# Kernel optimization log

Hardware: AMD Instinct MI355X
Metric: run time of the kernel (lower is better)

The kernel has to match this reference:

```python
import jax, jax.numpy as jnp
import numpy as np

N_NODES = 100000
N_EDGES = 1600000
F_IN = 92
E_IN = 50
D = 64
N_LAYERS = 3
N_GRAPHS = 512
BN_EPS = 1e-5


def setup_inputs() -> dict:
    key = jax.random.key(0)
    ks = jax.random.split(key, 24)
    s = 0.05
    inp = {
        'x': jax.random.normal(ks[0], (N_NODES, F_IN), jnp.float32),
        'edge_index': jax.random.randint(ks[1], (2, N_EDGES), 0, N_NODES, jnp.int64),
        'edge_attr': jax.random.normal(ks[2], (N_EDGES, E_IN), jnp.float32),
        'batch_idx': jnp.sort(jax.random.randint(ks[3], (N_NODES,), 0, N_GRAPHS, jnp.int64)),
        'pre_w': jax.random.normal(ks[4], (F_IN, D), jnp.float32) * s,
        'pre_b': jax.random.normal(ks[5], (D,), jnp.float32) * s,
        'Wk': jax.random.normal(ks[6], (N_LAYERS, D, D), jnp.float32) * s,
        'bk': jax.random.normal(ks[7], (N_LAYERS, D), jnp.float32) * s,
        'Wq': jax.random.normal(ks[8], (N_LAYERS, D, D), jnp.float32) * s,
        'bq': jax.random.normal(ks[9], (N_LAYERS, D), jnp.float32) * s,
        'Wv': jax.random.normal(ks[10], (N_LAYERS, D, D), jnp.float32) * s,
        'bv': jax.random.normal(ks[11], (N_LAYERS, D), jnp.float32) * s,
        'We': jax.random.normal(ks[12], (N_LAYERS, E_IN, D), jnp.float32) * s,
        'Wskip': jax.random.normal(ks[13], (N_LAYERS, D, D), jnp.float32) * s,
        'conv_bias': jax.random.normal(ks[14], (N_LAYERS, D), jnp.float32) * s,
        'bn_gamma': jnp.ones((N_LAYERS, D), jnp.float32),
        'bn_beta': jnp.zeros((N_LAYERS, D), jnp.float32),
        'post_w': jax.random.normal(ks[15], (D, D), jnp.float32) * s,
        'post_b': jax.random.normal(ks[16], (D,), jnp.float32) * s,
        'out_w': jax.random.normal(ks[17], (D, 1), jnp.float32) * s,
        'out_b': jax.random.normal(ks[18], (1,), jnp.float32) * s,
        'num_graphs': N_GRAPHS,
    }
    return inp


def _forward(x, edge_index, edge_attr, batch_idx, pre_w, pre_b, Wk, bk, Wq, bq, Wv, bv,
             We, Wskip, conv_bias, bn_gamma, bn_beta, post_w, post_b, out_w, out_b, num_graphs):
    n_nodes = x.shape[0]
    src, dst = edge_index[0], edge_index[1]  # j -> i, aggregate at i=dst
    # pre-FC + silu
    h = jax.nn.silu(x @ pre_w + pre_b)
    for l in range(Wk.shape[0]):
        # ResGatedGraphConv: node-level projections first (dense GEMMs)
        k = h @ Wk[l] + bk[l]   # key, used at target i
        q = h @ Wq[l] + bq[l]   # query, used at source j
        v = h @ Wv[l] + bv[l]   # value, used at source j
        e = edge_attr @ We[l]   # [E, D] edge embedding (no bias)
        # gather-gate-scatter over edges
        gate = jax.nn.silu((k[dst] + e) + (q[src] + e))  # act = silu
        msg = gate * (v[src] + e)                         # [E, D]
        agg = jax.ops.segment_sum(msg, dst, num_segments=n_nodes)
        h = agg + h @ Wskip[l] + conv_bias[l]
        # BatchNorm1d (training-mode batch stats, biased variance)
        mean = jnp.mean(h, axis=0)
        var = jnp.var(h, axis=0)
        h = (h - mean) * jax.lax.rsqrt(var + BN_EPS) * bn_gamma[l] + bn_beta[l]
        # dropout_rate = 0.0 -> no-op
    # global_mean_pool (early)
    sums = jax.ops.segment_sum(h, batch_idx, num_segments=num_graphs)
    cnts = jax.ops.segment_sum(jnp.ones((n_nodes,), h.dtype), batch_idx, num_segments=num_graphs)
    g = sums / jnp.maximum(cnts, 1.0)[:, None]
    g = jax.nn.silu(g @ post_w + post_b)
    out = g @ out_w + out_b  # [G, 1]
    return out.reshape(-1)


def reference(x, edge_index, edge_attr, batch_idx, pre_w, pre_b, Wk, bk, Wq, bq, Wv, bv,
              We, Wskip, conv_bias, bn_gamma, bn_beta, post_w, post_b, out_w, out_b, num_graphs):
    return _forward(x, edge_index, edge_attr, batch_idx, pre_w, pre_b, Wk, bk, Wq, bq, Wv, bv,
                    We, Wskip, conv_bias, bn_gamma, bn_beta, post_w, post_b, out_w, out_b, num_graphs)
```

## Files before the change

### kernel.cpp

```cpp
#include <hip/hip_runtime.h>
#include <math.h>

#define N_NODES 100000
#define N_EDGES 1600000
#define F_IN 92
#define E_IN 50
#define D 64
#define N_LAYERS 3
#define N_GRAPHS 512
#define BN_EPS 1e-5f

#define SCAN_BLK 1024
#define SCAN_NCH ((N_NODES + SCAN_BLK - 1) / SCAN_BLK)
#define EMB_TILE 256

__device__ __forceinline__ float silu_f(float x) {
    return x / (1.0f + __expf(-x));
}

__device__ __forceinline__ float bcast_f(float v, int lane) {
    return __int_as_float(__builtin_amdgcn_readlane(__float_as_int(v), lane));
}

__global__ __launch_bounds__(256) void deg_within_kernel(
    const int* __restrict__ dst, int* __restrict__ deg, int* __restrict__ within) {
    for (int e = blockIdx.x * 256 + threadIdx.x; e < N_EDGES; e += gridDim.x * 256)
        within[e] = atomicAdd(&deg[dst[e]], 1);
}

__global__ __launch_bounds__(SCAN_BLK) void scan_sum_kernel(
    const int* __restrict__ deg, int* __restrict__ partials) {
    int b = blockIdx.x, t = threadIdx.x;
    int i = b * SCAN_BLK + t;
    int v = (i < N_NODES) ? deg[i] : 0;
    __shared__ int wsum[16];
    for (int off = 32; off > 0; off >>= 1) v += __shfl_down(v, off);
    if ((t & 63) == 0) wsum[t >> 6] = v;
    __syncthreads();
    if (t < 16) {
        int s = wsum[t];
        for (int off = 8; off > 0; off >>= 1) s += __shfl_down(s, off);
        if (t == 0) partials[b] = s;
    }
}

__global__ __launch_bounds__(128) void scan_part_kernel(int* __restrict__ partials) {
    int t = threadIdx.x;
    __shared__ int sh[128];
    sh[t] = (t < SCAN_NCH) ? partials[t] : 0;
    __syncthreads();
    for (int off = 1; off < 128; off <<= 1) {
        int v = (t >= off) ? sh[t - off] : 0;
        __syncthreads();
        sh[t] += v;
        __syncthreads();
    }
    if (t < SCAN_NCH) partials[t] = (t == 0) ? 0 : sh[t - 1];
}

__global__ __launch_bounds__(SCAN_BLK) void scan_write_kernel(
    const int* __restrict__ deg, const int* __restrict__ partials,
    int* __restrict__ row_start, int* __restrict__ cursor) {
    int b = blockIdx.x, t = threadIdx.x;
    int i = b * SCAN_BLK + t;
    int v = (i < N_NODES) ? deg[i] : 0;
    __shared__ int sh[SCAN_BLK];
    sh[t] = v;
    __syncthreads();
    for (int off = 1; off < SCAN_BLK; off <<= 1) {
        int x = (t >= off) ? sh[t - off] : 0;
        __syncthreads();
        sh[t] += x;
        __syncthreads();
    }
    int excl = partials[b] + sh[t] - v;
    if (i < N_NODES) { row_start[i] = excl; cursor[i] = excl; }
    if (i == N_NODES - 1) row_start[N_NODES] = excl + v;
}

__global__ __launch_bounds__(256) void pos_fin_kernel(
    const int* __restrict__ srcIdx, const int* __restrict__ dst,
    const int* __restrict__ row_start, int* __restrict__ pos_arr,
    int* __restrict__ src_s) {
    for (int e = blockIdx.x * 256 + threadIdx.x; e < N_EDGES; e += gridDim.x * 256) {
        int p = row_start[dst[e]] + pos_arr[e];
        pos_arr[e] = p;
        src_s[p] = srcIdx[e];
    }
}

__global__ __launch_bounds__(256) void scatter_kernel(
    const int* __restrict__ dst, int* __restrict__ cursor,
    int* __restrict__ csr) {
    for (int e = blockIdx.x * 256 + threadIdx.x; e < N_EDGES; e += gridDim.x * 256) {
        int pos = atomicAdd(&cursor[dst[e]], 1);
        csr[pos] = e;
    }
}

template <int STRIDE>
__global__ __launch_bounds__(256) void scatter_perm_kernel(
    const int* __restrict__ srcIdx, const int* __restrict__ dstIdx,
    const float* __restrict__ ea, int* __restrict__ cursor,
    float* __restrict__ ea_s, int* __restrict__ src_s) {
    int d = threadIdx.x;
    int e = blockIdx.x * 4 + threadIdx.y;
    if (e >= N_EDGES) return;
    int pos = 0;
    if (d == 0) pos = atomicAdd(&cursor[dstIdx[e]], 1);
    pos = __builtin_amdgcn_readlane(pos, 0);
    if (d == 0) src_s[pos] = srcIdx[e];
    if (d < E_IN) ea_s[(long)pos * STRIDE + d] = ea[(long)e * E_IN + d];
}

__global__ __launch_bounds__(256) void pre_fc_kernel(
    const float* __restrict__ x, const float* __restrict__ w,
    const float* __restrict__ b, float* __restrict__ h) {
    __shared__ float xs[4][F_IN];
    int d = threadIdx.x, yy = threadIdx.y;
    int node = blockIdx.x * 4 + yy;
    if (node < N_NODES) {
        const float* xrow = x + (long)node * F_IN;
        for (int i = d; i < F_IN; i += 64) xs[yy][i] = xrow[i];
    }
    __syncthreads();
    if (node >= N_NODES) return;
    float acc = b[d];
#pragma unroll 4
    for (int i = 0; i < F_IN; ++i) acc = fmaf(xs[yy][i], w[i * D + d], acc);
    h[(long)node * D + d] = silu_f(acc);
}

template <bool BN>
__global__ __launch_bounds__(256) void proj_kernel(
    const float* __restrict__ hin, const float* __restrict__ stats,
    const float* __restrict__ gamma, const float* __restrict__ beta,
    const float* __restrict__ Wk, const float* __restrict__ bk,
    const float* __restrict__ Wq, const float* __restrict__ bq,
    const float* __restrict__ Wv, const float* __restrict__ bv,
    const float* __restrict__ Ws, const float* __restrict__ cbias,
    float* __restrict__ ko, float* __restrict__ qo, float* __restrict__ vo,
    float* __restrict__ hnew) {
    __shared__ float hs[4][D];
    int d = threadIdx.x, yy = threadIdx.y;
    int node = blockIdx.x * 4 + yy;
    if (node < N_NODES) {
        float xv = hin[(long)node * D + d];
        if (BN) {
            const float invN = 1.0f / (float)N_NODES;
            float mean = stats[d] * invN;
            float var = stats[D + d] * invN - mean * mean;
            float sc = rsqrtf(var + BN_EPS) * gamma[d];
            xv = (xv - mean) * sc + beta[d];
        }
        hs[yy][d] = xv;
    }
    __syncthreads();
    if (node >= N_NODES) return;
    float ak = bk[d], aq = bq[d], av = bv[d], as = cbias[d];
#pragma unroll 8
    for (int i = 0; i < D; ++i) {
        float hv = hs[yy][i];
        ak = fmaf(hv, Wk[i * D + d], ak);
        aq = fmaf(hv, Wq[i * D + d], aq);
        av = fmaf(hv, Wv[i * D + d], av);
        as = fmaf(hv, Ws[i * D + d], as);
    }
    long off = (long)node * D + d;
    ko[off] = ak; qo[off] = aq; vo[off] = av; hnew[off] = as;
}

__global__ __launch_bounds__(256) void edge_emb_perm_kernel(
    const float* __restrict__ ea, const int* __restrict__ pos_arr,
    const float* __restrict__ We, float* __restrict__ em) {
    __shared__ float tile[EMB_TILE * E_IN];
    int t = threadIdx.x;
    long e0 = (long)blockIdx.x * EMB_TILE;
    const float2* g = (const float2*)(ea + e0 * E_IN);
    float2* l2 = (float2*)tile;
#pragma unroll
    for (int k = 0; k < (EMB_TILE * E_IN) / 2; k += 256)
        l2[k + t] = g[k + t];
    int pos = pos_arr[e0 + t];
    __syncthreads();
    const float* row = tile + t * E_IN;
    float acc[D];
#pragma unroll
    for (int d = 0; d < D; ++d) acc[d] = 0.f;
#pragma unroll 5
    for (int i = 0; i < E_IN; ++i) {
        float ev = row[i];
#pragma unroll
        for (int d = 0; d < D; ++d) acc[d] = fmaf(ev, We[i * D + d], acc[d]);
    }
    float* out = em + (long)pos * D;
#pragma unroll
    for (int d = 0; d < D; d += 4)
        *reinterpret_cast<float4*>(out + d) =
            make_float4(acc[d], acc[d + 1], acc[d + 2], acc[d + 3]);
}

__global__ __launch_bounds__(256) void gather_em_kernel(
    const float* __restrict__ em, const int* __restrict__ src_s,
    const int* __restrict__ row_start,
    const float* __restrict__ kb, const float* __restrict__ qb,
    const float* __restrict__ vb, float* __restrict__ hnew) {
    int d = threadIdx.x;
    int node = blockIdx.x * 4 + threadIdx.y;
    if (node >= N_NODES) return;
    int lo = row_start[node], hi = row_start[node + 1];
    if (lo >= hi) return;
    float kv = kb[(long)node * D + d];
    float acc = 0.f;
    for (int base = lo; base < hi; base += 64) {
        int cnt = min(hi - base, 64);
        int s_l = 0;
        if (d < cnt) s_l = src_s[base + d];
        int s0 = __builtin_amdgcn_readlane(s_l, 0);
        float q_c = qb[(long)s0 * D + d];
        float v_c = vb[(long)s0 * D + d];
        float e_c = em[(long)base * D + d];
        float q_n = 0.f, v_n = 0.f, e_n = 0.f;
        if (cnt > 1) {
            int s1 = __builtin_amdgcn_readlane(s_l, 1);
            q_n = qb[(long)s1 * D + d];
            v_n = vb[(long)s1 * D + d];
            e_n = em[(long)(base + 1) * D + d];
        }
        for (int j = 0; j < cnt; ++j) {
            float q_2 = 0.f, v_2 = 0.f, e_2 = 0.f;
            if (j + 2 < cnt) {
                int s2 = __builtin_amdgcn_readlane(s_l, j + 2);
                q_2 = qb[(long)s2 * D + d];
                v_2 = vb[(long)s2 * D + d];
                e_2 = em[(long)(base + j + 2) * D + d];
            }
            float gate = silu_f(kv + q_c + 2.0f * e_c);
            acc = fmaf(gate, v_c + e_c, acc);
            q_c = q_n; v_c = v_n; e_c = e_n;
            q_n = q_2; v_n = v_2; e_n = e_2;
        }
    }
    long off = (long)node * D + d;
    hnew[off] += acc;
}

template <bool PERM>
__global__ __launch_bounds__(256) void gather_kernel(
    const float* __restrict__ ea, const int* __restrict__ srcArr,
    const int* __restrict__ csr, const int* __restrict__ row_start,
    const float* __restrict__ We,
    const float* __restrict__ kb, const float* __restrict__ qb,
    const float* __restrict__ vb, float* __restrict__ hnew) {
    int d = threadIdx.x;
    int node = blockIdx.x * 4 + threadIdx.y;
    if (node >= N_NODES) return;
    float WeReg[E_IN];
#pragma unroll
    for (int i = 0; i < E_IN; ++i) WeReg[i] = We[i * D + d];
    int lo = row_start[node], hi = row_start[node + 1];
    float kv = kb[(long)node * D + d];
    float acc = 0.f;
    for (int base = lo; base < hi; base += 64) {
        int cnt = min(hi - base, 64);
        int e_l = 0, s_l = 0;
        if (d < cnt) {
            int p = base + d;
            e_l = PERM ? p : csr[p];
            s_l = PERM ? srcArr[p] : srcArr[e_l];
        }
        int s_c = __builtin_amdgcn_readlane(s_l, 0);
        int r_c = PERM ? base : __builtin_amdgcn_readlane(e_l, 0);
        float q_c = qb[(long)s_c * D + d];
        float v_c = vb[(long)s_c * D + d];
        float e_c = (d < E_IN) ? ea[(long)r_c * E_IN + d] : 0.f;
        for (int j = 0; j < cnt; ++j) {
            float q_n = 0.f, v_n = 0.f, e_n = 0.f;
            if (j + 1 < cnt) {
                int s_n = __builtin_amdgcn_readlane(s_l, j + 1);
                int r_n = PERM ? (base + j + 1) : __builtin_amdgcn_readlane(e_l, j + 1);
                q_n = qb[(long)s_n * D + d];
                v_n = vb[(long)s_n * D + d];
                e_n = (d < E_IN) ? ea[(long)r_n * E_IN + d] : 0.f;
            }
            float ed0 = 0.f, ed1 = 0.f;
#pragma unroll
            for (int i = 0; i < E_IN; i += 2) {
                ed0 = fmaf(bcast_f(e_c, i), WeReg[i], ed0);
                ed1 = fmaf(bcast_f(e_c, i + 1), WeReg[i + 1], ed1);
            }
            float ed = ed0 + ed1;
            float gate = silu_f(kv + q_c + 2.0f * ed);
            acc = fmaf(gate, v_c + ed, acc);
            q_c = q_n; v_c = v_n; e_c = e_n;
        }
    }
    long off = (long)node * D + d;
    hnew[off] += acc;
}

__global__ __launch_bounds__(256) void bn_stats_kernel(
    const float* __restrict__ hnew, float* __restrict__ stats) {
    int d = threadIdx.x, yy = threadIdx.y;
    float s = 0.f, s2 = 0.f;
    for (int n = blockIdx.x * 4 + yy; n < N_NODES; n += gridDim.x * 4) {
        float v = hnew[(long)n * D + d];
        s += v;
        s2 = fmaf(v, v, s2);
    }
    __shared__ float ls[4][D], ls2[4][D];
    ls[yy][d] = s; ls2[yy][d] = s2;
    __syncthreads();
    if (yy == 0) {
        atomicAdd(&stats[d],     ls[0][d] + ls[1][d] + ls[2][d] + ls[3][d]);
        atomicAdd(&stats[D + d], ls2[0][d] + ls2[1][d] + ls2[2][d] + ls2[3][d]);
    }
}

__global__ __launch_bounds__(256) void graph_bounds_kernel(
    const int* __restrict__ batch, int* __restrict__ start) {
    int n = blockIdx.x * 256 + threadIdx.x;
    if (n >= N_NODES) return;
    int b = batch[n];
    if (n == 0) {
        for (int g = 0; g <= b; ++g) start[g] = 0;
    } else {
        int p = batch[n - 1];
        for (int g = p + 1; g <= b; ++g) start[g] = n;
    }
    if (n == N_NODES - 1) {
        for (int g = b + 1; g <= N_GRAPHS; ++g) start[g] = N_NODES;
    }
}

__global__ __launch_bounds__(256) void pool_head_kernel(
    const float* __restrict__ hnew, const int* __restrict__ start,
    const float* __restrict__ stats, const float* __restrict__ gamma,
    const float* __restrict__ beta,
    const float* __restrict__ pw, const float* __restrict__ pb,
    const float* __restrict__ ow, const float* __restrict__ ob,
    float* __restrict__ out) {
    int g = blockIdx.x;
    int d = threadIdx.x, yy = threadIdx.y;
    int lo = start[g], hi = start[g + 1];
    float s = 0.f;
    for (int n = lo + yy; n < hi; n += 4) s += hnew[(long)n * D + d];
    __shared__ float ls[4][D];
    ls[yy][d] = s;
    __syncthreads();
    __shared__ float grow[D];
    if (yy == 0) {
        float tot = ls[0][d] + ls[1][d] + ls[2][d] + ls[3][d];
        float gd = 0.f;
        if (hi > lo) {
            float m = tot / (float)(hi - lo);
            const float invN = 1.0f / (float)N_NODES;
            float mean = stats[d] * invN;
            float var = stats[D + d] * invN - mean * mean;
            float sc = rsqrtf(var + BN_EPS) * gamma[d];
            gd = (m - mean) * sc + beta[d];
        }
        grow[d] = gd;
    }
    __syncthreads();
    if (yy != 0) return;
    float accp = pb[d];
#pragma unroll 8
    for (int i = 0; i < D; ++i) accp = fmaf(grow[i], pw[i * D + d], accp);
    float sv = silu_f(accp) * ow[d];
    for (int off = 32; off > 0; off >>= 1) sv += __shfl_down(sv, off);
    if (d == 0) out[g] = sv + ob[0];
}

extern "C" void kernel_launch(void* const* d_in, const int* in_sizes, int n_in,
                              void* d_out, int out_size, void* d_ws, size_t ws_size,
                              hipStream_t stream) {
    const float* x        = (const float*)d_in[0];
    const int*   ei       = (const int*)d_in[1];
    const float* ea       = (const float*)d_in[2];
    const int*   batch    = (const int*)d_in[3];
    const float* pre_w    = (const float*)d_in[4];
    const float* pre_b    = (const float*)d_in[5];
    const float* Wk       = (const float*)d_in[6];
    const float* bk       = (const float*)d_in[7];
    const float* Wq       = (const float*)d_in[8];
    const float* bq       = (const float*)d_in[9];
    const float* Wv       = (const float*)d_in[10];
    const float* bv       = (const float*)d_in[11];
    const float* We       = (const float*)d_in[12];
    const float* Wskip    = (const float*)d_in[13];
    const float* conv_bias= (const float*)d_in[14];
    const float* bn_gamma = (const float*)d_in[15];
    const float* bn_beta  = (const float*)d_in[16];
    const float* post_w   = (const float*)d_in[17];
    const float* post_b   = (const float*)d_in[18];
    const float* out_w    = (const float*)d_in[19];
    const float* out_b    = (const float*)d_in[20];

    char* base = (char*)d_ws;
    float* ws = (float*)d_ws;
    const size_t NH = (size_t)N_NODES * D;
    float* bufA  = ws;
    float* bufB  = ws + NH;
    float* kb    = ws + 2 * NH;
    float* qb    = ws + 3 * NH;
    float* vb    = ws + 4 * NH;
    float* stats = ws + 5 * NH;
    int*   start     = (int*)(stats + 6 * D);
    int*   deg       = start + (N_GRAPHS + 1);
    int*   row_start = deg + N_NODES;
    int*   cursor    = row_start + (N_NODES + 1);
    int*   partials  = cursor + N_NODES;
    int*   posb      = partials + 128;

    size_t off_e = (size_t)((char*)(posb + N_EDGES) - base);
    off_e = (off_e + 255) & ~(size_t)255;

    size_t em_offF = (off_e + (size_t)N_EDGES * sizeof(int) + 255) & ~(size_t)255;
    size_t needF = em_offF + (size_t)N_EDGES * D * sizeof(float);
    bool tierF = ws_size >= needF;
    size_t src_off1 = off_e + (size_t)N_EDGES * E_IN * sizeof(float);
    bool tier1 = !tierF && (ws_size >= src_off1 + (size_t)N_EDGES * sizeof(int));

    const int* srcIdx = ei;
    const int* dstIdx = ei + N_EDGES;

    dim3 blk(64, 4);
    const int NB_N = (N_NODES + 3) / 4;

    hipMemsetAsync(deg, 0, N_NODES * sizeof(int), stream);
    hipMemsetAsync(stats, 0, 6 * D * sizeof(float), stream);
    deg_within_kernel<<<1024, 256, 0, stream>>>(dstIdx, deg, posb);
    scan_sum_kernel<<<SCAN_NCH, SCAN_BLK, 0, stream>>>(deg, partials);
    scan_part_kernel<<<1, 128, 0, stream>>>(partials);
    scan_write_kernel<<<SCAN_NCH, SCAN_BLK, 0, stream>>>(deg, partials, row_start, cursor);

    int*   srcF = (int*)(base + off_e);
    float* emF  = (float*)(base + em_offF);
    float* ea1  = (float*)(base + off_e);
    int*   src1 = (int*)(base + src_off1);

    if (tierF) {
        pos_fin_kernel<<<1024, 256, 0, stream>>>(srcIdx, dstIdx, row_start, posb, srcF);
    } else if (tier1) {
        scatter_perm_kernel<E_IN><<<(N_EDGES + 3) / 4, blk, 0, stream>>>(
            srcIdx, dstIdx, ea, cursor, ea1, src1);
    } else {
        scatter_kernel<<<1024, 256, 0, stream>>>(dstIdx, cursor, posb);
    }

    pre_fc_kernel<<<NB_N, blk, 0, stream>>>(x, pre_w, pre_b, bufA);

    float* hin = bufA;
    float* hout = bufB;
    for (int l = 0; l < N_LAYERS; ++l) {
        if (l == 0)
            proj_kernel<false><<<NB_N, blk, 0, stream>>>(
                hin, nullptr, nullptr, nullptr,
                Wk + l * D * D, bk + l * D, Wq + l * D * D, bq + l * D,
                Wv + l * D * D, bv + l * D, Wskip + l * D * D, conv_bias + l * D,
                kb, qb, vb, hout);
        else
            proj_kernel<true><<<NB_N, blk, 0, stream>>>(
                hin, stats + (l - 1) * 2 * D, bn_gamma + (l - 1) * D, bn_beta + (l - 1) * D,
                Wk + l * D * D, bk + l * D, Wq + l * D * D, bq + l * D,
                Wv + l * D * D, bv + l * D, Wskip + l * D * D, conv_bias + l * D,
                kb, qb, vb, hout);
        if (tierF) {
            edge_emb_perm_kernel<<<N_EDGES / EMB_TILE, 256, 0, stream>>>(
                ea, posb, We + l * E_IN * D, emF);
            gather_em_kernel<<<NB_N, blk, 0, stream>>>(
                emF, srcF, row_start, kb, qb, vb, hout);
        } else if (tier1) {
            gather_kernel<true><<<NB_N, blk, 0, stream>>>(
                ea1, src1, posb, row_start, We + l * E_IN * D, kb, qb, vb, hout);
        } else {
            gather_kernel<false><<<NB_N, blk, 0, stream>>>(
                ea, srcIdx, posb, row_start, We + l * E_IN * D, kb, qb, vb, hout);
        }
        bn_stats_kernel<<<256, blk, 0, stream>>>(hout, stats + l * 2 * D);
        float* t = hin; hin = hout; hout = t;
    }

    graph_bounds_kernel<<<(N_NODES + 255) / 256, 256, 0, stream>>>(batch, start);
    pool_head_kernel<<<N_GRAPHS, blk, 0, stream>>>(
        hin, start, stats + (N_LAYERS - 1) * 2 * D,
        bn_gamma + (N_LAYERS - 1) * D, bn_beta + (N_LAYERS - 1) * D,
        post_w, post_b, out_w, out_b, (float*)d_out);
}
```

Baseline: 2.501 ms.

## Make edge embedding persistent with register-prefetched tiles; deepen gather prefetch

The edge-embedding kernel becomes a persistent grid of 1536 blocks with 128-edge tiles. Each block prefetches the next tile's edge attributes and permutation index into registers while it computes the current tile. The inner GEMV loop now reads edge features as float2 pairs. The gather kernel's software prefetch depth grows from 2 to 3 edges, giving the random q/v/em loads more latency hiding at the cost of extra registers.

After: 3.083 ms. +23.3%, slower.

```diff
diff --git a/kernel.cpp b/kernel.cpp
--- a/kernel.cpp
+++ b/kernel.cpp
@@ -12,7 +12,9 @@
 
 #define SCAN_BLK 1024
 #define SCAN_NCH ((N_NODES + SCAN_BLK - 1) / SCAN_BLK)
-#define EMB_TILE 256
+#define EMB_TILE 128
+#define EMB_NT (N_EDGES / EMB_TILE)
+#define EMB_GRID 1536
 
 __device__ __forceinline__ float silu_f(float x) {
     return x / (1.0f + __expf(-x));
@@ -170,34 +172,53 @@
     ko[off] = ak; qo[off] = aq; vo[off] = av; hnew[off] = as;
 }
 
-__global__ __launch_bounds__(256) void edge_emb_perm_kernel(
+__global__ __launch_bounds__(128) void edge_emb_perm_kernel(
     const float* __restrict__ ea, const int* __restrict__ pos_arr,
     const float* __restrict__ We, float* __restrict__ em) {
     __shared__ float tile[EMB_TILE * E_IN];
     int t = threadIdx.x;
-    long e0 = (long)blockIdx.x * EMB_TILE;
-    const float2* g = (const float2*)(ea + e0 * E_IN);
-    float2* l2 = (float2*)tile;
-#pragma unroll
-    for (int k = 0; k < (EMB_TILE * E_IN) / 2; k += 256)
-        l2[k + t] = g[k + t];
-    int pos = pos_arr[e0 + t];
-    __syncthreads();
-    const float* row = tile + t * E_IN;
-    float acc[D];
-#pragma unroll
-    for (int d = 0; d < D; ++d) acc[d] = 0.f;
-#pragma unroll 5
-    for (int i = 0; i < E_IN; ++i) {
-        float ev = row[i];
-#pragma unroll
-        for (int d = 0; d < D; ++d) acc[d] = fmaf(ev, We[i * D + d], acc[d]);
-    }
-    float* out = em + (long)pos * D;
-#pragma unroll
-    for (int d = 0; d < D; d += 4)
-        *reinterpret_cast<float4*>(out + d) =
-            make_float4(acc[d], acc[d + 1], acc[d + 2], acc[d + 3]);
+    float2 reg[E_IN / 2];
+    int pos_pref;
+    {
+        long e0 = (long)blockIdx.x * EMB_TILE;
+        const float2* g = (const float2*)(ea + e0 * E_IN);
+#pragma unroll
+        for (int k = 0; k < E_IN / 2; ++k) reg[k] = g[k * EMB_TILE + t];
+        pos_pref = pos_arr[e0 + t];
+    }
+    for (int ti = blockIdx.x; ti < EMB_NT; ti += EMB_GRID) {
+        float2* l2 = (float2*)tile;
+#pragma unroll
+        for (int k = 0; k < E_IN / 2; ++k) l2[k * EMB_TILE + t] = reg[k];
+        int pos = pos_pref;
+        __syncthreads();
+        int nxt = ti + EMB_GRID;
+        if (nxt < EMB_NT) {
+            long e0 = (long)nxt * EMB_TILE;
+            const float2* g = (const float2*)(ea + e0 * E_IN);
+#pragma unroll
+            for (int k = 0; k < E_IN / 2; ++k) reg[k] = g[k * EMB_TILE + t];
+            pos_pref = pos_arr[e0 + t];
+        }
+        const float* row = tile + t * E_IN;
+        float acc[D];
+#pragma unroll
+        for (int d = 0; d < D; ++d) acc[d] = 0.f;
+#pragma unroll
+        for (int i = 0; i < E_IN; i += 2) {
+            float2 ev = *reinterpret_cast<const float2*>(row + i);
+#pragma unroll
+            for (int d = 0; d < D; ++d) acc[d] = fmaf(ev.x, We[i * D + d], acc[d]);
+#pragma unroll
+            for (int d = 0; d < D; ++d) acc[d] = fmaf(ev.y, We[(i + 1) * D + d], acc[d]);
+        }
+        float* out = em + (long)pos * D;
+#pragma unroll
+        for (int d = 0; d < D; d += 4)
+            *reinterpret_cast<float4*>(out + d) =
+                make_float4(acc[d], acc[d + 1], acc[d + 2], acc[d + 3]);
+        __syncthreads();
+    }
 }
 
 __global__ __launch_bounds__(256) void gather_em_kernel(
@@ -216,29 +237,36 @@
         int cnt = min(hi - base, 64);
         int s_l = 0;
         if (d < cnt) s_l = src_s[base + d];
-        int s0 = __builtin_amdgcn_readlane(s_l, 0);
-        float q_c = qb[(long)s0 * D + d];
-        float v_c = vb[(long)s0 * D + d];
-        float e_c = em[(long)base * D + d];
-        float q_n = 0.f, v_n = 0.f, e_n = 0.f;
+        float q0 = 0.f, v0 = 0.f, e0 = 0.f;
+        float q1 = 0.f, v1 = 0.f, e1 = 0.f;
+        float q2 = 0.f, v2 = 0.f, e2 = 0.f;
+        {
+            int s = __builtin_amdgcn_readlane(s_l, 0);
+            q0 = qb[(long)s * D + d]; v0 = vb[(long)s * D + d];
+            e0 = em[(long)base * D + d];
+        }
         if (cnt > 1) {
-            int s1 = __builtin_amdgcn_readlane(s_l, 1);
-            q_n = qb[(long)s1 * D + d];
-            v_n = vb[(long)s1 * D + d];
-            e_n = em[(long)(base + 1) * D + d];
+            int s = __builtin_amdgcn_readlane(s_l, 1);
+            q1 = qb[(long)s * D + d]; v1 = vb[(long)s * D + d];
+            e1 = em[(long)(base + 1) * D + d];
+        }
+        if (cnt > 2) {
+            int s = __builtin_amdgcn_readlane(s_l, 2);
+            q2 = qb[(long)s * D + d]; v2 = vb[(long)s * D + d];
+            e2 = em[(long)(base + 2) * D + d];
         }
         for (int j = 0; j < cnt; ++j) {
-            float q_2 = 0.f, v_2 = 0.f, e_2 = 0.f;
-            if (j + 2 < cnt) {
-                int s2 = __builtin_amdgcn_readlane(s_l, j + 2);
-                q_2 = qb[(long)s2 * D + d];
-                v_2 = vb[(long)s2 * D + d];
-                e_2 = em[(long)(base + j + 2) * D + d];
+            float q3 = 0.f, v3 = 0.f, e3 = 0.f;
+            if (j + 3 < cnt) {
+                int s = __builtin_amdgcn_readlane(s_l, j + 3);
+                q3 = qb[(long)s * D + d]; v3 = vb[(long)s * D + d];
+                e3 = em[(long)(base + j + 3) * D + d];
             }
-            float gate = silu_f(kv + q_c + 2.0f * e_c);
-            acc = fmaf(gate, v_c + e_c, acc);
-            q_c = q_n; v_c = v_n; e_c = e_n;
-            q_n = q_2; v_n = v_2; e_n = e_2;
+            float gate = silu_f(kv + q0 + 2.0f * e0);
+            acc = fmaf(gate, v0 + e0, acc);
+            q0 = q1; v0 = v1; e0 = e1;
+            q1 = q2; v1 = v2; e1 = e2;
+            q2 = q3; v2 = v3; e2 = e3;
         }
     }
     long off = (long)node * D + d;
@@ -467,7 +495,7 @@
                 Wv + l * D * D, bv + l * D, Wskip + l * D * D, conv_bias + l * D,
                 kb, qb, vb, hout);
         if (tierF) {
-            edge_emb_perm_kernel<<<N_EDGES / EMB_TILE, 256, 0, stream>>>(
+            edge_emb_perm_kernel<<<EMB_GRID, 128, 0, stream>>>(
                 ea, posb, We + l * E_IN * D, emF);
             gather_em_kernel<<<NB_N, blk, 0, stream>>>(
                 emF, srcF, row_start, kb, qb, vb, hout);
```
